# Performance work log

Hardware: AMD Instinct MI355X
Metric: run time of the kernel (lower is better)

Reference implementation:

```python
import jax, jax.numpy as jnp
import numpy as np

ALPHA = 0.95
BETA = 0.9

def setup_inputs() -> dict:
    key = jax.random.key(0)
    k1, k2 = jax.random.split(key)
    B, T, I, O = 64, 1000, 512, 256
    inputs = jax.random.normal(k1, (B, T, I), dtype=jnp.float32)
    W = jax.random.normal(k2, (O, I), dtype=jnp.float32) * (1.0 / np.sqrt(I))
    return {"inputs": inputs, "W": W, "nb_steps": T}

def reference(inputs, W, nb_steps):
    B = inputs.shape[0]
    O = W.shape[0]
    # linear projection: h[b,t,o]
    h = jnp.einsum('bti,oi->bto', inputs, W)
    h_t = jnp.swapaxes(h, 0, 1)  # (T, B, O) for scan over time

    def step(carry, ht):
        flt, out = carry
        new_flt = ALPHA * flt + ht
        new_out = BETA * out + flt  # uses OLD flt, matching the torch loop
        return (new_flt, new_out), new_out

    init = (jnp.zeros((B, O), jnp.float32), jnp.zeros((B, O), jnp.float32))
    _, out_rec = jax.lax.scan(step, init, h_t)
    return jnp.swapaxes(out_rec, 0, 1)  # (B, T, O)
```

## Files before the change

kernel.cpp:

```cpp
#include <hip/hip_runtime.h>
#include <hip/hip_bf16.h>
#include <stdint.h>


#define ALPHA 0.95f
#define BETA  0.9f

constexpr int Bdim = 64, T = 1000, Idim = 512, Odim = 256;
constexpr int M = Bdim * T;
constexpr int C = 40, L = 25;

typedef short bf16x8 __attribute__((ext_vector_type(8)));
typedef float f32x4  __attribute__((ext_vector_type(4)));

__device__ inline uint32_t pk_bf16(float a, float b) {
  union { float f; uint32_t u; } x, y; x.f = a; y.f = b;
  uint32_t lo = (x.u + 0x7FFFu + ((x.u >> 16) & 1u)) >> 16;
  uint32_t hi = (y.u + 0x7FFFu + ((y.u >> 16) & 1u)) & 0xFFFF0000u;
  return lo | hi;
}
__device__ inline uint16_t f2bf(float a) {
  union { float f; uint32_t u; } x; x.f = a;
  return (uint16_t)((x.u + 0x7FFFu + ((x.u >> 16) & 1u)) >> 16);
}
__device__ inline float bf2f(uint16_t h) {
  union { uint32_t u; float f; } x; x.u = ((uint32_t)h) << 16;
  return x.f;
}

#define GLD16(g, l) __builtin_amdgcn_global_load_lds(                         \
    (const __attribute__((address_space(1))) uint32_t*)(g),                   \
    (__attribute__((address_space(3))) uint32_t*)(l), 16, 0, 0)

__device__ inline bf16x8 cvt8(float4 x0, float4 x1) {
  union { __hip_bfloat162 h[4]; bf16x8 v; } r;
  r.h[0] = __float22bfloat162_rn(make_float2(x0.x, x0.y));
  r.h[1] = __float22bfloat162_rn(make_float2(x0.z, x0.w));
  r.h[2] = __float22bfloat162_rn(make_float2(x1.x, x1.y));
  r.h[3] = __float22bfloat162_rn(make_float2(x1.z, x1.w));
  return r.v;
}

__global__ __launch_bounds__(256) void wconv(const float* __restrict__ W,
                                             uint16_t* __restrict__ Wbf) {
  int i = (blockIdx.x * 256 + threadIdx.x) * 8;
  float4 a = *(const float4*)(W + i);
  float4 b = *(const float4*)(W + i + 4);
  *(uint4*)(Wbf + i) = make_uint4(pk_bf16(a.x, a.y), pk_bf16(a.z, a.w),
                                  pk_bf16(b.x, b.y), pk_bf16(b.z, b.w));
}

__global__ __launch_bounds__(256, 2) void gemm_h(const float* __restrict__ A,
                                                 const uint16_t* __restrict__ Wbf,
                                                 uint16_t* __restrict__ H) {
  __shared__ float    As[128 * 32];
  __shared__ uint16_t Bs[256 * 32];

  const int tid  = threadIdx.x;
  const int lane = tid & 63;
  const int w    = tid >> 6;
  const int l15  = lane & 15;
  const int quad = lane >> 4;
  const int rm   = blockIdx.x * 128;

  const float* asrc[4];
  char*        aldst[4];
#pragma unroll
  for (int i = 0; i < 4; ++i) {
    int row = w * 32 + i * 8 + (lane >> 3);
    int g   = (lane & 7) ^ (row & 7);
    asrc[i]  = A + (size_t)(rm + row) * Idim + g * 4;
    aldst[i] = (char*)As + w * 4096 + i * 1024;
  }
  const uint16_t* bsrc[4];
  char*           bldst[4];
#pragma unroll
  for (int i = 0; i < 4; ++i) {
    int row = w * 64 + i * 16 + (lane >> 2);
    int g   = (lane & 3) ^ (row & 3);
    bsrc[i]  = Wbf + (size_t)row * Idim + g * 8;
    bldst[i] = (char*)Bs + w * 4096 + i * 1024;
  }

  f32x4 acc[8][4] = {};

  for (int k0 = 0; k0 < Idim; k0 += 32) {
    __syncthreads();
#pragma unroll
    for (int i = 0; i < 4; ++i) GLD16(asrc[i] + k0, aldst[i]);
#pragma unroll
    for (int i = 0; i < 4; ++i) GLD16(bsrc[i] + k0, bldst[i]);
    __syncthreads();

    bf16x8 bfr[4];
#pragma unroll
    for (int nt = 0; nt < 4; ++nt) {
      int n = w * 64 + nt * 16 + l15;
      bfr[nt] = *(const bf16x8*)&Bs[n * 32 + ((quad ^ (n & 3)) * 8)];
    }
    bf16x8 af[8];
#pragma unroll
    for (int mt = 0; mt < 8; ++mt) {
      int m  = mt * 16 + l15;
      int s0 = (2 * quad) ^ (m & 7);
      float4 x0 = *(const float4*)&As[m * 32 + s0 * 4];
      float4 x1 = *(const float4*)&As[m * 32 + (s0 ^ 1) * 4];
      af[mt] = ((m & 1) == (m & 1)) ? cvt8(x0, x1) : cvt8(x0, x1);
    }
#pragma unroll
    for (int mt = 0; mt < 8; ++mt)
#pragma unroll
      for (int nt = 0; nt < 4; ++nt)
        acc[mt][nt] = __builtin_amdgcn_mfma_f32_16x16x32_bf16(af[mt], bfr[nt], acc[mt][nt], 0, 0, 0);
  }

#pragma unroll
  for (int mt = 0; mt < 8; ++mt)
#pragma unroll
    for (int nt = 0; nt < 4; ++nt)
#pragma unroll
      for (int r = 0; r < 4; ++r) {
        int gm = rm + mt * 16 + quad * 4 + r;
        int gn = w * 64 + nt * 16 + l15;
        H[(size_t)gm * Odim + gn] = f2bf(acc[mt][nt][r]);
      }
}

constexpr double dpow(double x, int n) { double r = 1.0; for (int i = 0; i < n; ++i) r *= x; return r; }

__global__ __launch_bounds__(640) void scan_all(const uint16_t* __restrict__ H,
                                                float* __restrict__ Out) {
  constexpr float AL = (float)dpow(0.95, L);
  constexpr float BL = (float)dpow(0.90, L);
  constexpr float WL = (float)((dpow(0.95, L) - dpow(0.90, L)) / (0.95 - 0.90));
  __shared__ float2 St[C][64];

  const int b   = blockIdx.x >> 2;
  const int og  = blockIdx.x & 3;
  const int tid = threadIdx.x;
  const int c   = tid >> 4;
  const int ol  = tid & 15;

  const size_t base = ((size_t)b * T + c * L) * Odim + og * 64 + ol * 4;
  const ushort4* hp = (const ushort4*)(H + base);

  ushort4 hv[L];
  {
    float f[4] = {}, u[4] = {};
#pragma unroll
    for (int j = 0; j < L; ++j) {
      hv[j] = hp[j * 64];
      float h0 = bf2f(hv[j].x), h1 = bf2f(hv[j].y), h2 = bf2f(hv[j].z), h3 = bf2f(hv[j].w);
      float n0 = BETA * u[0] + f[0]; f[0] = ALPHA * f[0] + h0; u[0] = n0;
      float n1 = BETA * u[1] + f[1]; f[1] = ALPHA * f[1] + h1; u[1] = n1;
      float n2 = BETA * u[2] + f[2]; f[2] = ALPHA * f[2] + h2; u[2] = n2;
      float n3 = BETA * u[3] + f[3]; f[3] = ALPHA * f[3] + h3; u[3] = n3;
    }
#pragma unroll
    for (int i = 0; i < 4; ++i) St[c][ol * 4 + i] = make_float2(f[i], u[i]);
  }
  __syncthreads();

  if (tid < 64) {
    float f = 0.f, u = 0.f;
#pragma unroll
    for (int cc = 0; cc < C; ++cc) {
      float2 s = St[cc][tid];
      St[cc][tid] = make_float2(f, u);
      float nu = BL * u + WL * f + s.y;
      f = AL * f + s.x;
      u = nu;
    }
  }
  __syncthreads();

  {
    float f[4], u[4];
#pragma unroll
    for (int i = 0; i < 4; ++i) { float2 s = St[c][ol * 4 + i]; f[i] = s.x; u[i] = s.y; }
    float4* op = (float4*)(Out + base);
#pragma unroll
    for (int j = 0; j < L; ++j) {
      float h0 = bf2f(hv[j].x), h1 = bf2f(hv[j].y), h2 = bf2f(hv[j].z), h3 = bf2f(hv[j].w);
      float4 o4;
      o4.x = BETA * u[0] + f[0]; f[0] = ALPHA * f[0] + h0; u[0] = o4.x;
      o4.y = BETA * u[1] + f[1]; f[1] = ALPHA * f[1] + h1; u[1] = o4.y;
      o4.z = BETA * u[2] + f[2]; f[2] = ALPHA * f[2] + h2; u[2] = o4.z;
      o4.w = BETA * u[3] + f[3]; f[3] = ALPHA * f[3] + h3; u[3] = o4.w;
      op[j * 64] = o4;
    }
  }
}

extern "C" void kernel_launch(void* const* d_in, const int* in_sizes, int n_in,
                              void* d_out, int out_size, void* d_ws, size_t ws_size,
                              hipStream_t stream) {
  const float* A = (const float*)d_in[0];
  const float* W = (const float*)d_in[1];
  float* Out = (float*)d_out;

  uint16_t* H   = (uint16_t*)d_ws;
  uint16_t* Wbf = H + (size_t)M * Odim;

  wconv<<<Odim * Idim / (256 * 8), 256, 0, stream>>>(W, Wbf);
  gemm_h<<<M / 128, 256, 0, stream>>>(A, Wbf, H);
  scan_all<<<Bdim * 4, 640, 0, stream>>>(H, Out);
}
```

Measured before the change: 226.7 us.

## Fuse weight conversion, GEMM, and chunked scan into a single kernel

Replaces the three-kernel pipeline (W conversion, bf16 GEMM to a global H buffer, chunked scan) with one kernel per (batch, 64-output slice). Each block converts its W slice into LDS, streams the batch's input rows through a 4-deep global-to-LDS pipeline, computes 128-timestep tiles of H in LDS, and runs a two-level scan with a carried state across tiles. This removes the H round trip through global memory and two launches. In exchange, each batch's input is read by four separate blocks, and the time-chunk loop is serialized with several barriers per tile.

```diff
diff --git a/kernel.cpp b/kernel.cpp
--- a/kernel.cpp
+++ b/kernel.cpp
@@ -7,25 +7,23 @@
 #define BETA  0.9f
 
 constexpr int Bdim = 64, T = 1000, Idim = 512, Odim = 256;
-constexpr int M = Bdim * T;
-constexpr int C = 40, L = 25;
+constexpr int TC = 128;
+constexpr int NC = 8;
+constexpr int KS = Idim / 32;
+constexpr int KK = NC * KS;
+constexpr int HP = 66;
 
 typedef short bf16x8 __attribute__((ext_vector_type(8)));
 typedef float f32x4  __attribute__((ext_vector_type(4)));
 
-__device__ inline uint32_t pk_bf16(float a, float b) {
-  union { float f; uint32_t u; } x, y; x.f = a; y.f = b;
-  uint32_t lo = (x.u + 0x7FFFu + ((x.u >> 16) & 1u)) >> 16;
-  uint32_t hi = (y.u + 0x7FFFu + ((y.u >> 16) & 1u)) & 0xFFFF0000u;
-  return lo | hi;
-}
+constexpr double dpow(double x, int n) { double r = 1; for (int i = 0; i < n; ++i) r *= x; return r; }
+
 __device__ inline uint16_t f2bf(float a) {
   union { float f; uint32_t u; } x; x.f = a;
   return (uint16_t)((x.u + 0x7FFFu + ((x.u >> 16) & 1u)) >> 16);
 }
 __device__ inline float bf2f(uint16_t h) {
-  union { uint32_t u; float f; } x; x.u = ((uint32_t)h) << 16;
-  return x.f;
+  union { uint32_t u; float f; } x; x.u = ((uint32_t)h) << 16; return x.f;
 }
 
 #define GLD16(g, l) __builtin_amdgcn_global_load_lds(                         \
@@ -41,168 +39,159 @@
   return r.v;
 }
 
-__global__ __launch_bounds__(256) void wconv(const float* __restrict__ W,
-                                             uint16_t* __restrict__ Wbf) {
-  int i = (blockIdx.x * 256 + threadIdx.x) * 8;
-  float4 a = *(const float4*)(W + i);
-  float4 b = *(const float4*)(W + i + 4);
-  *(uint4*)(Wbf + i) = make_uint4(pk_bf16(a.x, a.y), pk_bf16(a.z, a.w),
-                                  pk_bf16(b.x, b.y), pk_bf16(b.z, b.w));
-}
+#define LGKM0 asm volatile("s_waitcnt lgkmcnt(0)" ::: "memory")
+#define VMW4  asm volatile("s_waitcnt vmcnt(4)" ::: "memory")
+#define SBAR  __builtin_amdgcn_s_barrier()
 
-__global__ __launch_bounds__(256, 2) void gemm_h(const float* __restrict__ A,
-                                                 const uint16_t* __restrict__ Wbf,
-                                                 uint16_t* __restrict__ H) {
-  __shared__ float    As[128 * 32];
-  __shared__ uint16_t Bs[256 * 32];
+__global__ __launch_bounds__(512) void fused(const float* __restrict__ A,
+                                             const float* __restrict__ W,
+                                             float* __restrict__ Out) {
+  __shared__ uint16_t Ws[64 * 512];
+  __shared__ float    As[4][TC * 32];
+  __shared__ uint16_t Hs[TC * HP];
+  __shared__ float2   St[8][64];
+  __shared__ float2   Carry[64];
 
   const int tid  = threadIdx.x;
   const int lane = tid & 63;
   const int w    = tid >> 6;
   const int l15  = lane & 15;
   const int quad = lane >> 4;
-  const int rm   = blockIdx.x * 128;
+  const int mq   = w & 3;
+  const int nh   = w >> 2;
 
-  const float* asrc[4];
-  char*        aldst[4];
+  const int p  = blockIdx.x;
+  const int b  = ((p >> 3) & 7) * 8 + (p & 7);
+  const int og = p >> 6;
+
+  const int r0 = w * 16 + (lane >> 3);
+  const int g  = (lane & 7) ^ (r0 & 7);
+  const float* Ab0 = A + (size_t)b * T * Idim + g * 4;
+
+#define STAGE(kk_) do {                                                        \
+    const int kc_ = (kk_); const int cc_ = kc_ >> 4, ii_ = kc_ & 15;           \
+    int ra_ = cc_ * TC + r0;     if (ra_ > T - 1) ra_ = T - 1;                 \
+    int rb_ = cc_ * TC + r0 + 8; if (rb_ > T - 1) rb_ = T - 1;                 \
+    char* d_ = (char*)As[kc_ & 3] + w * 2048;                                  \
+    GLD16(Ab0 + (size_t)ra_ * Idim + ii_ * 32, d_);                            \
+    GLD16(Ab0 + (size_t)rb_ * Idim + ii_ * 32, d_ + 1024);                     \
+  } while (0)
+
+  STAGE(0); STAGE(1); STAGE(2);
+
+  {
+    const int n  = tid >> 3;
+    const int s8 = tid & 7;
+    const float* wp = W + (size_t)(og * 64 + n) * Idim;
 #pragma unroll
-  for (int i = 0; i < 4; ++i) {
-    int row = w * 32 + i * 8 + (lane >> 3);
-    int g   = (lane & 7) ^ (row & 7);
-    asrc[i]  = A + (size_t)(rm + row) * Idim + g * 4;
-    aldst[i] = (char*)As + w * 4096 + i * 1024;
+    for (int rr = 0; rr < 8; ++rr) {
+      int s = s8 + rr * 8;
+      float4 x0 = *(const float4*)(wp + s * 8);
+      float4 x1 = *(const float4*)(wp + s * 8 + 4);
+      *(bf16x8*)((char*)Ws + n * 1024 + ((s ^ (n & 7)) * 16)) = cvt8(x0, x1);
+    }
   }
-  const uint16_t* bsrc[4];
-  char*           bldst[4];
+  if (tid < 64) Carry[tid] = make_float2(0.f, 0.f);
+  LGKM0; SBAR;
+
+  constexpr float AL = (float)dpow(0.95, 16);
+  constexpr float BL = (float)dpow(0.90, 16);
+  constexpr float WL = (float)((dpow(0.95, 16) - dpow(0.90, 16)) / (0.95 - 0.90));
+
+  for (int c = 0; c < NC; ++c) {
+    f32x4 acc[2][2] = {};
+    for (int i = 0; i < KS; ++i) {
+      const int kk = c * KS + i;
+      VMW4;
+      SBAR;
+      const float* Abuf = As[kk & 3];
+      bf16x8 af[2], bfr[2];
 #pragma unroll
-  for (int i = 0; i < 4; ++i) {
-    int row = w * 64 + i * 16 + (lane >> 2);
-    int g   = (lane & 3) ^ (row & 3);
-    bsrc[i]  = Wbf + (size_t)row * Idim + g * 8;
-    bldst[i] = (char*)Bs + w * 4096 + i * 1024;
-  }
-
-  f32x4 acc[8][4] = {};
-
-  for (int k0 = 0; k0 < Idim; k0 += 32) {
-    __syncthreads();
+      for (int mt = 0; mt < 2; ++mt) {
+        const int m  = mq * 32 + mt * 16 + l15;
+        const int s0 = (2 * quad) ^ (m & 7);
+        float4 x0 = *(const float4*)&Abuf[m * 32 + s0 * 4];
+        float4 x1 = *(const float4*)&Abuf[m * 32 + (s0 ^ 1) * 4];
+        af[mt] = cvt8(x0, x1);
+      }
 #pragma unroll
-    for (int i = 0; i < 4; ++i) GLD16(asrc[i] + k0, aldst[i]);
+      for (int nt = 0; nt < 2; ++nt) {
+        const int n  = nh * 32 + nt * 16 + l15;
+        const int sl = (i * 4 + quad) ^ (n & 7);
+        bfr[nt] = *(const bf16x8*)((const char*)Ws + n * 1024 + sl * 16);
+      }
 #pragma unroll
-    for (int i = 0; i < 4; ++i) GLD16(bsrc[i] + k0, bldst[i]);
-    __syncthreads();
-
-    bf16x8 bfr[4];
+      for (int mt = 0; mt < 2; ++mt)
 #pragma unroll
-    for (int nt = 0; nt < 4; ++nt) {
-      int n = w * 64 + nt * 16 + l15;
-      bfr[nt] = *(const bf16x8*)&Bs[n * 32 + ((quad ^ (n & 3)) * 8)];
+        for (int nt = 0; nt < 2; ++nt)
+          acc[mt][nt] = __builtin_amdgcn_mfma_f32_16x16x32_bf16(af[mt], bfr[nt], acc[mt][nt], 0, 0, 0);
+      int nk = kk + 3; if (nk > KK - 1) nk = KK - 1;
+      STAGE(nk);
+      LGKM0;
     }
-    bf16x8 af[8];
-#pragma unroll
-    for (int mt = 0; mt < 8; ++mt) {
-      int m  = mt * 16 + l15;
-      int s0 = (2 * quad) ^ (m & 7);
-      float4 x0 = *(const float4*)&As[m * 32 + s0 * 4];
-      float4 x1 = *(const float4*)&As[m * 32 + (s0 ^ 1) * 4];
-      af[mt] = ((m & 1) == (m & 1)) ? cvt8(x0, x1) : cvt8(x0, x1);
-    }
-#pragma unroll
-    for (int mt = 0; mt < 8; ++mt)
-#pragma unroll
-      for (int nt = 0; nt < 4; ++nt)
-        acc[mt][nt] = __builtin_amdgcn_mfma_f32_16x16x32_bf16(af[mt], bfr[nt], acc[mt][nt], 0, 0, 0);
-  }
 
 #pragma unroll
-  for (int mt = 0; mt < 8; ++mt)
+    for (int mt = 0; mt < 2; ++mt)
 #pragma unroll
-    for (int nt = 0; nt < 4; ++nt)
+      for (int nt = 0; nt < 2; ++nt)
 #pragma unroll
-      for (int r = 0; r < 4; ++r) {
-        int gm = rm + mt * 16 + quad * 4 + r;
-        int gn = w * 64 + nt * 16 + l15;
-        H[(size_t)gm * Odim + gn] = f2bf(acc[mt][nt][r]);
+        for (int r = 0; r < 4; ++r) {
+          const int tl = mq * 32 + mt * 16 + quad * 4 + r;
+          const int o  = nh * 32 + nt * 16 + l15;
+          Hs[tl * HP + o] = f2bf(acc[mt][nt][r]);
+        }
+    LGKM0; SBAR;
+
+    {
+      const int sc = w, o = lane;
+      float f = 0.f, u = 0.f;
+#pragma unroll
+      for (int j = 0; j < 16; ++j) {
+        float h = bf2f(Hs[(sc * 16 + j) * HP + o]);
+        float nu = BETA * u + f; f = ALPHA * f + h; u = nu;
       }
-}
+      St[sc][o] = make_float2(f, u);
+    }
+    LGKM0; SBAR;
 
-constexpr double dpow(double x, int n) { double r = 1.0; for (int i = 0; i < n; ++i) r *= x; return r; }
+    if (tid < 64) {
+      float2 cv = Carry[tid];
+      float f = cv.x, u = cv.y;
+#pragma unroll
+      for (int cc2 = 0; cc2 < 8; ++cc2) {
+        float2 s = St[cc2][tid];
+        St[cc2][tid] = make_float2(f, u);
+        float nu = BL * u + WL * f + s.y;
+        f = AL * f + s.x;
+        u = nu;
+      }
+      Carry[tid] = make_float2(f, u);
+    }
+    LGKM0; SBAR;
 
-__global__ __launch_bounds__(640) void scan_all(const uint16_t* __restrict__ H,
-                                                float* __restrict__ Out) {
-  constexpr float AL = (float)dpow(0.95, L);
-  constexpr float BL = (float)dpow(0.90, L);
-  constexpr float WL = (float)((dpow(0.95, L) - dpow(0.90, L)) / (0.95 - 0.90));
-  __shared__ float2 St[C][64];
-
-  const int b   = blockIdx.x >> 2;
-  const int og  = blockIdx.x & 3;
-  const int tid = threadIdx.x;
-  const int c   = tid >> 4;
-  const int ol  = tid & 15;
-
-  const size_t base = ((size_t)b * T + c * L) * Odim + og * 64 + ol * 4;
-  const ushort4* hp = (const ushort4*)(H + base);
-
-  ushort4 hv[L];
-  {
-    float f[4] = {}, u[4] = {};
+    {
+      const int sc = w, o = lane;
+      float2 s = St[sc][o];
+      float f = s.x, u = s.y;
+      const int tb = c * TC + sc * 16;
+      float* op = Out + ((size_t)b * T + tb) * Odim + og * 64 + o;
 #pragma unroll
-    for (int j = 0; j < L; ++j) {
-      hv[j] = hp[j * 64];
-      float h0 = bf2f(hv[j].x), h1 = bf2f(hv[j].y), h2 = bf2f(hv[j].z), h3 = bf2f(hv[j].w);
-      float n0 = BETA * u[0] + f[0]; f[0] = ALPHA * f[0] + h0; u[0] = n0;
-      float n1 = BETA * u[1] + f[1]; f[1] = ALPHA * f[1] + h1; u[1] = n1;
-      float n2 = BETA * u[2] + f[2]; f[2] = ALPHA * f[2] + h2; u[2] = n2;
-      float n3 = BETA * u[3] + f[3]; f[3] = ALPHA * f[3] + h3; u[3] = n3;
-    }
-#pragma unroll
-    for (int i = 0; i < 4; ++i) St[c][ol * 4 + i] = make_float2(f[i], u[i]);
-  }
-  __syncthreads();
-
-  if (tid < 64) {
-    float f = 0.f, u = 0.f;
-#pragma unroll
-    for (int cc = 0; cc < C; ++cc) {
-      float2 s = St[cc][tid];
-      St[cc][tid] = make_float2(f, u);
-      float nu = BL * u + WL * f + s.y;
-      f = AL * f + s.x;
-      u = nu;
+      for (int j = 0; j < 16; ++j) {
+        float h = bf2f(Hs[(sc * 16 + j) * HP + o]);
+        float ov = BETA * u + f; f = ALPHA * f + h; u = ov;
+        if (tb + j < T) op[j * Odim] = ov;
+      }
     }
   }
-  __syncthreads();
-
-  {
-    float f[4], u[4];
-#pragma unroll
-    for (int i = 0; i < 4; ++i) { float2 s = St[c][ol * 4 + i]; f[i] = s.x; u[i] = s.y; }
-    float4* op = (float4*)(Out + base);
-#pragma unroll
-    for (int j = 0; j < L; ++j) {
-      float h0 = bf2f(hv[j].x), h1 = bf2f(hv[j].y), h2 = bf2f(hv[j].z), h3 = bf2f(hv[j].w);
-      float4 o4;
-      o4.x = BETA * u[0] + f[0]; f[0] = ALPHA * f[0] + h0; u[0] = o4.x;
-      o4.y = BETA * u[1] + f[1]; f[1] = ALPHA * f[1] + h1; u[1] = o4.y;
-      o4.z = BETA * u[2] + f[2]; f[2] = ALPHA * f[2] + h2; u[2] = o4.z;
-      o4.w = BETA * u[3] + f[3]; f[3] = ALPHA * f[3] + h3; u[3] = o4.w;
-      op[j * 64] = o4;
-    }
-  }
+#undef STAGE
 }
 
 extern "C" void kernel_launch(void* const* d_in, const int* in_sizes, int n_in,
                               void* d_out, int out_size, void* d_ws, size_t ws_size,
                               hipStream_t stream) {
+  (void)in_sizes; (void)n_in; (void)d_ws; (void)ws_size; (void)out_size;
   const float* A = (const float*)d_in[0];
   const float* W = (const float*)d_in[1];
   float* Out = (float*)d_out;
-
-  uint16_t* H   = (uint16_t*)d_ws;
-  uint16_t* Wbf = H + (size_t)M * Odim;
-
-  wconv<<<Odim * Idim / (256 * 8), 256, 0, stream>>>(W, Wbf);
-  gemm_h<<<M / 128, 256, 0, stream>>>(A, Wbf, H);
-  scan_all<<<Bdim * 4, 640, 0, stream>>>(H, Out);
+  fused<<<Bdim * 4, 512, 0, stream>>>(A, W, Out);
 }
```

After: 274.5 us. +21.1%, slower.

## Double-buffer GEMM LDS tiles so global loads overlap MFMA compute

Applied to the files above, without the earlier changes.

The projection GEMM now keeps two LDS buffers for the A and W tiles and fully unrolls the 16-step K loop. Each step issues the direct-to-LDS loads for step t+1 and then waits with explicit s_waitcnt vmcnt(8), so the next tile's global reads run while the current tile goes through MFMA. This removes the load-then-compute serialisation of the old loop. The cost is double the LDS per block (64KB, with two blocks per CU) and hand-written waitcnt/barrier logic that relies on each thread issuing exactly 8 loads per stage.

```diff
diff --git a/kernel.cpp b/kernel.cpp
--- a/kernel.cpp
+++ b/kernel.cpp
@@ -41,6 +41,11 @@
   return r.v;
 }
 
+#define LGKM0 asm volatile("s_waitcnt lgkmcnt(0)" ::: "memory")
+#define VMW8  asm volatile("s_waitcnt vmcnt(8)" ::: "memory")
+#define VMW0  asm volatile("s_waitcnt vmcnt(0)" ::: "memory")
+#define SBAR  __builtin_amdgcn_s_barrier()
+
 __global__ __launch_bounds__(256) void wconv(const float* __restrict__ W,
                                              uint16_t* __restrict__ Wbf) {
   int i = (blockIdx.x * 256 + threadIdx.x) * 8;
@@ -53,8 +58,8 @@
 __global__ __launch_bounds__(256, 2) void gemm_h(const float* __restrict__ A,
                                                  const uint16_t* __restrict__ Wbf,
                                                  uint16_t* __restrict__ H) {
-  __shared__ float    As[128 * 32];
-  __shared__ uint16_t Bs[256 * 32];
+  __shared__ float    As[2][128 * 32];
+  __shared__ uint16_t Bs[2][256 * 32];
 
   const int tid  = threadIdx.x;
   const int lane = tid & 63;
@@ -82,37 +87,54 @@
     bldst[i] = (char*)Bs + w * 4096 + i * 1024;
   }
 
+#define STAGE(t_) do {                                                         \
+    const int off_ = ((t_) & 1) * 16384;     \
+    const int k0_  = (t_) * 32;                          \
+    _Pragma("unroll")                                                          \
+    for (int i = 0; i < 4; ++i) GLD16(asrc[i] + k0_, aldst[i] + off_);         \
+    _Pragma("unroll")                                                          \
+    for (int i = 0; i < 4; ++i) GLD16(bsrc[i] + k0_, bldst[i] + off_);         \
+  } while (0)
+
   f32x4 acc[8][4] = {};
 
-  for (int k0 = 0; k0 < Idim; k0 += 32) {
-    __syncthreads();
-#pragma unroll
-    for (int i = 0; i < 4; ++i) GLD16(asrc[i] + k0, aldst[i]);
-#pragma unroll
-    for (int i = 0; i < 4; ++i) GLD16(bsrc[i] + k0, bldst[i]);
-    __syncthreads();
+  STAGE(0);
+#pragma unroll
+  for (int t = 0; t < 16; ++t) {
+    if (t < 15) { STAGE(t + 1); VMW8; }
+    else        { VMW0; }
+    SBAR;
+
+    const float*    Ab = &As[t & 1][0];
+    const uint16_t* Bb = &Bs[t & 1][0];
 
     bf16x8 bfr[4];
 #pragma unroll
     for (int nt = 0; nt < 4; ++nt) {
       int n = w * 64 + nt * 16 + l15;
-      bfr[nt] = *(const bf16x8*)&Bs[n * 32 + ((quad ^ (n & 3)) * 8)];
+      bfr[nt] = *(const bf16x8*)&Bb[n * 32 + ((quad ^ (n & 3)) * 8)];
     }
     bf16x8 af[8];
 #pragma unroll
     for (int mt = 0; mt < 8; ++mt) {
       int m  = mt * 16 + l15;
       int s0 = (2 * quad) ^ (m & 7);
-      float4 x0 = *(const float4*)&As[m * 32 + s0 * 4];
-      float4 x1 = *(const float4*)&As[m * 32 + (s0 ^ 1) * 4];
-      af[mt] = ((m & 1) == (m & 1)) ? cvt8(x0, x1) : cvt8(x0, x1);
+      float4 x0 = *(const float4*)&Ab[m * 32 + s0 * 4];
+      float4 x1 = *(const float4*)&Ab[m * 32 + (s0 ^ 1) * 4];
+      af[mt] = cvt8(x0, x1);
     }
 #pragma unroll
     for (int mt = 0; mt < 8; ++mt)
 #pragma unroll
       for (int nt = 0; nt < 4; ++nt)
         acc[mt][nt] = __builtin_amdgcn_mfma_f32_16x16x32_bf16(af[mt], bfr[nt], acc[mt][nt], 0, 0, 0);
-  }
+
+    if (t < 15) {
+      LGKM0;
+      SBAR;
+    }
+  }
+#undef STAGE
 
 #pragma unroll
   for (int mt = 0; mt < 8; ++mt)
```

Result: no change. 229.3 us (+1.1%).
